# Performance work log

Measured on AMD Instinct MI355X. Metric: run time of the kernel, lower is better.

## Reference

```python
import jax, jax.numpy as jnp
import numpy as np

# fatigue class -> emotion target distribution; row 3 is the uniform fallback
_TABLE = np.array([
    [0.05, 0.02, 0.03, 0.4, 0.05, 0.4, 0.05],
    [0.05, 0.05, 0.05, 0.05, 0.3, 0.05, 0.45],
    [0.1, 0.15, 0.2, 0.02, 0.35, 0.03, 0.15],
    [1.0 / 7.0] * 7,
], dtype=np.float32)

B = 4_000_000

def setup_inputs() -> dict:
    key = jax.random.key(0)
    k1, k2, k3 = jax.random.split(key, 3)
    fatigue_logits = jax.random.normal(k1, (B, 3), dtype=jnp.float32)
    emotion_logits = jax.random.normal(k2, (B, 7), dtype=jnp.float32)
    fatigue_targets = jax.random.randint(k3, (B,), 0, 4, dtype=jnp.int64)
    return {"fatigue_logits": fatigue_logits,
            "emotion_logits": emotion_logits,
            "fatigue_targets": fatigue_targets}

def reference(fatigue_logits, emotion_logits, fatigue_targets):
    eps = 1e-8
    table = jnp.asarray(_TABLE)
    # targets outside {0,1,2} map to the uniform row (index 3)
    idx = jnp.where((fatigue_targets >= 0) & (fatigue_targets <= 2), fatigue_targets, 3)
    target = table[idx]                      # [B, 7] gather from tiny LUT
    target = target + eps
    target = target / jnp.sum(target, axis=-1, keepdims=True)
    probs = jax.nn.softmax(emotion_logits, axis=-1)
    log_input = jnp.log(probs + eps)
    # F.kl_div(log_input, target, reduction='batchmean')
    kl = jnp.sum(target * (jnp.log(target) - log_input)) / target.shape[0]
    return kl
```

## Files before the change

### kernel.cpp

```cpp
#include <hip/hip_runtime.h>
#include <cmath>

struct KLC {
    float w0[7], w1[7], w2[7], w3[7];
    float cst0, cst1, cst2, cst3;
};

typedef __attribute__((ext_vector_type(4))) float f4;
typedef __attribute__((ext_vector_type(4))) int   i4;

__device__ __forceinline__ void row_part(
    float x0, float x1, float x2, float x3, float x4, float x5, float x6,
    int t, const KLC& kc, float& lin, float& Z)
{
    int c = ((unsigned)t <= 2u) ? t : 3;

    Z = __expf(x0) + __expf(x1) + __expf(x2) + __expf(x3)
      + __expf(x4) + __expf(x5) + __expf(x6);

    float d0 = fmaf(kc.w0[6], x6, fmaf(kc.w0[5], x5, fmaf(kc.w0[4], x4,
               fmaf(kc.w0[3], x3, fmaf(kc.w0[2], x2, fmaf(kc.w0[1], x1, kc.w0[0] * x0))))));
    float d1 = fmaf(kc.w1[6], x6, fmaf(kc.w1[5], x5, fmaf(kc.w1[4], x4,
               fmaf(kc.w1[3], x3, fmaf(kc.w1[2], x2, fmaf(kc.w1[1], x1, kc.w1[0] * x0))))));
    float d2 = fmaf(kc.w2[6], x6, fmaf(kc.w2[5], x5, fmaf(kc.w2[4], x4,
               fmaf(kc.w2[3], x3, fmaf(kc.w2[2], x2, fmaf(kc.w2[1], x1, kc.w2[0] * x0))))));
    float d3 = fmaf(kc.w3[6], x6, fmaf(kc.w3[5], x5, fmaf(kc.w3[4], x4,
               fmaf(kc.w3[3], x3, fmaf(kc.w3[2], x2, fmaf(kc.w3[1], x1, kc.w3[0] * x0))))));

    float dw = (c == 0) ? d0 : (c == 1) ? d1 : (c == 2) ? d2 : d3;
    float cs = (c == 0) ? kc.cst0 : (c == 1) ? kc.cst1 : (c == 2) ? kc.cst2 : kc.cst3;
    lin = cs - dw;
}

__device__ __forceinline__ float quad_kl(
    f4 c0, f4 c1, f4 c2, f4 c3, f4 c4, f4 c5, f4 c6, i4 tq, const KLC& kc)
{
    float l0, l1, l2, l3, Z0, Z1, Z2, Z3;
    row_part(c0.x, c0.y, c0.z, c0.w, c1.x, c1.y, c1.z, tq.x, kc, l0, Z0);
    row_part(c1.w, c2.x, c2.y, c2.z, c2.w, c3.x, c3.y, tq.y, kc, l1, Z1);
    row_part(c3.z, c3.w, c4.x, c4.y, c4.z, c4.w, c5.x, tq.z, kc, l2, Z2);
    row_part(c5.y, c5.z, c5.w, c6.x, c6.y, c6.z, c6.w, tq.w, kc, l3, Z3);
    return l0 + l1 + l2 + l3 + __logf((Z0 * Z1) * (Z2 * Z3));
}

__global__ __launch_bounds__(256) void kl_main(
    const float* __restrict__ logits,
    const int*   __restrict__ tgt,
    int noct,
    double* __restrict__ partial,
    KLC kc)
{
    const f4* __restrict__ lg = (const f4*)logits;
    const i4* __restrict__ tg = (const i4*)tgt;

    int tid = blockIdx.x * blockDim.x + threadIdx.x;
    float local = 0.0f;
    if (tid < noct) {
        long long b = (long long)tid * 14;
        f4 a0 = __builtin_nontemporal_load(&lg[b + 0]);
        f4 a1 = __builtin_nontemporal_load(&lg[b + 1]);
        f4 a2 = __builtin_nontemporal_load(&lg[b + 2]);
        f4 a3 = __builtin_nontemporal_load(&lg[b + 3]);
        f4 a4 = __builtin_nontemporal_load(&lg[b + 4]);
        f4 a5 = __builtin_nontemporal_load(&lg[b + 5]);
        f4 a6 = __builtin_nontemporal_load(&lg[b + 6]);
        f4 b0 = __builtin_nontemporal_load(&lg[b + 7]);
        f4 b1 = __builtin_nontemporal_load(&lg[b + 8]);
        f4 b2 = __builtin_nontemporal_load(&lg[b + 9]);
        f4 b3 = __builtin_nontemporal_load(&lg[b + 10]);
        f4 b4 = __builtin_nontemporal_load(&lg[b + 11]);
        f4 b5 = __builtin_nontemporal_load(&lg[b + 12]);
        f4 b6 = __builtin_nontemporal_load(&lg[b + 13]);
        i4 t0 = __builtin_nontemporal_load(&tg[(long long)tid * 2 + 0]);
        i4 t1 = __builtin_nontemporal_load(&tg[(long long)tid * 2 + 1]);

        local  = quad_kl(a0, a1, a2, a3, a4, a5, a6, t0, kc);
        local += quad_kl(b0, b1, b2, b3, b4, b5, b6, t1, kc);
    }

    #pragma unroll
    for (int off = 32; off > 0; off >>= 1)
        local += __shfl_down(local, off, 64);

    __shared__ float smem[4];
    int lane = threadIdx.x & 63;
    int wid  = threadIdx.x >> 6;
    if (lane == 0) smem[wid] = local;
    __syncthreads();
    if (threadIdx.x == 0)
        partial[blockIdx.x] = (double)(smem[0] + smem[1] + smem[2] + smem[3]);
}

__global__ __launch_bounds__(256) void kl_reduce(
    const float* __restrict__ logits,
    const int*   __restrict__ tgt,
    long long tail_start, int tail,
    const double* __restrict__ partial, int nb,
    float* __restrict__ out, int B, KLC kc)
{
    double s = 0.0;
    for (int i = threadIdx.x; i < nb; i += 256) s += partial[i];

    float tl = 0.0f;
    for (int r = threadIdx.x; r < tail; r += 256) {
        const float* x = logits + (tail_start + r) * 7;
        float lin, Z;
        row_part(x[0], x[1], x[2], x[3], x[4], x[5], x[6],
                 tgt[tail_start + r], kc, lin, Z);
        tl += lin + __logf(Z);
    }
    s += (double)tl;

    #pragma unroll
    for (int off = 32; off > 0; off >>= 1)
        s += __shfl_down(s, off, 64);

    __shared__ double smem[4];
    int lane = threadIdx.x & 63;
    int wid  = threadIdx.x >> 6;
    if (lane == 0) smem[wid] = s;
    __syncthreads();
    if (threadIdx.x == 0)
        out[0] = (float)((smem[0] + smem[1] + smem[2] + smem[3]) / (double)B);
}

extern "C" void kernel_launch(void* const* d_in, const int* in_sizes, int n_in,
                              void* d_out, int out_size, void* d_ws, size_t ws_size,
                              hipStream_t stream) {
    const float* emotion = (const float*)d_in[1];
    const int*   targets = (const int*)d_in[2];
    float*  out     = (float*)d_out;
    double* partial = (double*)d_ws;

    const int B = in_sizes[2];
    const int noct = B / 8;
    const int tail = B - noct * 8;
    const long long tail_start = (long long)noct * 8;

    int nb = (noct + 255) / 256;
    if ((size_t)nb * sizeof(double) > ws_size)
        nb = (int)(ws_size / sizeof(double));

    static const double T[4][7] = {
        {0.05, 0.02, 0.03, 0.4, 0.05, 0.4, 0.05},
        {0.05, 0.05, 0.05, 0.05, 0.3, 0.05, 0.45},
        {0.1, 0.15, 0.2, 0.02, 0.35, 0.03, 0.15},
        {1.0/7.0, 1.0/7.0, 1.0/7.0, 1.0/7.0, 1.0/7.0, 1.0/7.0, 1.0/7.0},
    };
    const double eps = 1e-8;
    KLC kc;
    float* wrows[4] = { kc.w0, kc.w1, kc.w2, kc.w3 };
    float* csts[4]  = { &kc.cst0, &kc.cst1, &kc.cst2, &kc.cst3 };
    for (int c = 0; c < 4; ++c) {
        double s = 0.0;
        for (int j = 0; j < 7; ++j) s += T[c][j] + eps;
        double cst = 0.0;
        for (int j = 0; j < 7; ++j) {
            double w = (T[c][j] + eps) / s;
            wrows[c][j] = (float)w;
            cst += w * std::log(w);
        }
        *csts[c] = (float)cst;
    }

    kl_main<<<nb, 256, 0, stream>>>(emotion, targets, noct, partial, kc);
    kl_reduce<<<1, 256, 0, stream>>>(emotion, targets, tail_start, tail,
                                     partial, nb, out, B, kc);
}
```

Before: 224.6 us.

## Stage logits through LDS with global_load_lds in a grid-stride wave loop

Replaces per-thread 16-float-vector register loads with a persistent grid-stride loop: each wave loads 256 rows of logits into LDS through direct global-to-LDS loads, fully coalesced, then reads them back per lane. The grid becomes a fixed 1280 blocks and each lane handles 4 rows per iteration instead of 8. The loop waits for each chunk's loads before computing, so nothing overlaps within a wave and latency hiding relies on occupancy. It also drops the nontemporal hints.

```diff
diff --git a/kernel.cpp b/kernel.cpp
--- a/kernel.cpp
+++ b/kernel.cpp
@@ -46,36 +46,46 @@
 __global__ __launch_bounds__(256) void kl_main(
     const float* __restrict__ logits,
     const int*   __restrict__ tgt,
-    int noct,
+    int nchunks,
     double* __restrict__ partial,
     KLC kc)
 {
+    __shared__ f4 lds[4 * 448 + 4];
+    const int lane = threadIdx.x & 63;
+    const int wave = threadIdx.x >> 6;
+    f4* const myl = &lds[wave * 448];
+
     const f4* __restrict__ lg = (const f4*)logits;
     const i4* __restrict__ tg = (const i4*)tgt;
 
-    int tid = blockIdx.x * blockDim.x + threadIdx.x;
+    const int gwave  = blockIdx.x * 4 + wave;
+    const int nwaves = gridDim.x * 4;
+
     float local = 0.0f;
-    if (tid < noct) {
-        long long b = (long long)tid * 14;
-        f4 a0 = __builtin_nontemporal_load(&lg[b + 0]);
-        f4 a1 = __builtin_nontemporal_load(&lg[b + 1]);
-        f4 a2 = __builtin_nontemporal_load(&lg[b + 2]);
-        f4 a3 = __builtin_nontemporal_load(&lg[b + 3]);
-        f4 a4 = __builtin_nontemporal_load(&lg[b + 4]);
-        f4 a5 = __builtin_nontemporal_load(&lg[b + 5]);
-        f4 a6 = __builtin_nontemporal_load(&lg[b + 6]);
-        f4 b0 = __builtin_nontemporal_load(&lg[b + 7]);
-        f4 b1 = __builtin_nontemporal_load(&lg[b + 8]);
-        f4 b2 = __builtin_nontemporal_load(&lg[b + 9]);
-        f4 b3 = __builtin_nontemporal_load(&lg[b + 10]);
-        f4 b4 = __builtin_nontemporal_load(&lg[b + 11]);
-        f4 b5 = __builtin_nontemporal_load(&lg[b + 12]);
-        f4 b6 = __builtin_nontemporal_load(&lg[b + 13]);
-        i4 t0 = __builtin_nontemporal_load(&tg[(long long)tid * 2 + 0]);
-        i4 t1 = __builtin_nontemporal_load(&tg[(long long)tid * 2 + 1]);
+    for (int ch = gwave; ch < nchunks; ch += nwaves) {
+        asm volatile("s_waitcnt lgkmcnt(0)" ::: "memory");
 
-        local  = quad_kl(a0, a1, a2, a3, a4, a5, a6, t0, kc);
-        local += quad_kl(b0, b1, b2, b3, b4, b5, b6, t1, kc);
+        const long long base4 = (long long)ch * 448;
+        #pragma unroll
+        for (int k = 0; k < 7; ++k) {
+            __builtin_amdgcn_global_load_lds(
+                (const __attribute__((address_space(1))) void*)(lg + base4 + k * 64 + lane),
+                (__attribute__((address_space(3))) void*)(myl + k * 64),
+                16, 0, 0);
+        }
+        i4 tq = tg[(long long)ch * 64 + lane];
+
+        asm volatile("s_waitcnt vmcnt(0)" ::: "memory");
+
+        f4 c0 = myl[lane * 7 + 0];
+        f4 c1 = myl[lane * 7 + 1];
+        f4 c2 = myl[lane * 7 + 2];
+        f4 c3 = myl[lane * 7 + 3];
+        f4 c4 = myl[lane * 7 + 4];
+        f4 c5 = myl[lane * 7 + 5];
+        f4 c6 = myl[lane * 7 + 6];
+
+        local += quad_kl(c0, c1, c2, c3, c4, c5, c6, tq, kc);
     }
 
     #pragma unroll
@@ -83,9 +93,7 @@
         local += __shfl_down(local, off, 64);
 
     __shared__ float smem[4];
-    int lane = threadIdx.x & 63;
-    int wid  = threadIdx.x >> 6;
-    if (lane == 0) smem[wid] = local;
+    if (lane == 0) smem[wave] = local;
     __syncthreads();
     if (threadIdx.x == 0)
         partial[blockIdx.x] = (double)(smem[0] + smem[1] + smem[2] + smem[3]);
@@ -133,11 +141,11 @@
     double* partial = (double*)d_ws;
 
     const int B = in_sizes[2];
-    const int noct = B / 8;
-    const int tail = B - noct * 8;
-    const long long tail_start = (long long)noct * 8;
+    const int nchunks = B / 256;
+    const int tail = B - nchunks * 256;
+    const long long tail_start = (long long)nchunks * 256;
 
-    int nb = (noct + 255) / 256;
+    int nb = 1280;
     if ((size_t)nb * sizeof(double) > ws_size)
         nb = (int)(ws_size / sizeof(double));
 
@@ -163,7 +171,7 @@
         *csts[c] = (float)cst;
     }
 
-    kl_main<<<nb, 256, 0, stream>>>(emotion, targets, noct, partial, kc);
+    kl_main<<<nb, 256, 0, stream>>>(emotion, targets, nchunks, partial, kc);
     kl_reduce<<<1, 256, 0, stream>>>(emotion, targets, tail_start, tail,
                                      partial, nb, out, B, kc);
 }
```

After: 196.1 us. 12.7% less time.
